# Performance work log

Hardware: AMD Instinct MI355X
Metric: run time of the kernel (lower is better)

## Reference

```python
import jax, jax.numpy as jnp
import numpy as np

E, D, H, B, S = 16, 1024, 256, 4, 4096  # num_splats, model_dim, ff_dim//num_splats, batch, seq_len


def setup_inputs() -> dict:
    key = jax.random.key(0)
    ks = jax.random.split(key, 8)
    s = 0.02  # init scale for stability
    return {
        "x": jax.random.normal(ks[0], (B, S, D), dtype=jnp.float32),
        "splat_id": jax.random.randint(ks[1], (S,), 0, E, dtype=jnp.int32),
        "W1": jax.random.normal(ks[2], (E, D, H), dtype=jnp.float32) * s,
        "b1": jnp.zeros((E, H), dtype=jnp.float32),
        "W2": jax.random.normal(ks[3], (E, H, D), dtype=jnp.float32) * s,
        "b2": jnp.zeros((E, D), dtype=jnp.float32),
        "Wg1": jax.random.normal(ks[4], (D, D), dtype=jnp.float32) * s,
        "bg1": jnp.zeros((D,), dtype=jnp.float32),
        "Wg2": jax.random.normal(ks[5], (D, D), dtype=jnp.float32) * s,
        "bg2": jnp.zeros((D,), dtype=jnp.float32),
    }


def reference(x, splat_id, W1, b1, W2, b2, Wg1, bg1, Wg2, bg2):
    # Splat-aware dispatch: token s is processed by expert splat_id[s].
    # Equivalent vectorized form: run every expert's small MLP, mask at the
    # hidden layer by expert assignment, and sum over experts (each token is
    # assigned to exactly one expert, matching the gather->MLP->scatter loop).
    nE = W1.shape[0]
    onehot = (splat_id[None, :] == jnp.arange(nE, dtype=splat_id.dtype)[:, None]).astype(x.dtype)  # [E,S]
    # hidden: [E,B,S,H]
    h = jax.nn.gelu(jnp.einsum('bsd,edh->ebsh', x, W1) + b1[:, None, None, :], approximate=False)
    h = h * onehot[:, None, :, None]  # zero tokens not routed to expert e
    routed = jnp.einsum('ebsh,ehd->bsd', h, W2)  # [B,S,D]
    routed = routed + jnp.einsum('es,ed->sd', onehot, b2)[None, :, :]  # per-token expert bias
    # global aggregator MLP (torch GELU default = exact erf form)
    g = jax.nn.gelu(routed @ Wg1 + bg1, approximate=False)
    return g @ Wg2 + bg2
```

## Files before the change

kernel.cpp:

```cpp
#include <hip/hip_runtime.h>


#define DEV __device__ __forceinline__

typedef float f32x4 __attribute__((ext_vector_type(4)));
typedef short short8 __attribute__((ext_vector_type(8)));

DEV unsigned short f2bf(float f) {
  unsigned u = __float_as_uint(f);
  u += 0x7fffu + ((u >> 16) & 1u);
  return (unsigned short)(u >> 16);
}

DEV void gload_lds16(const void* g, void* l) {
  __builtin_amdgcn_global_load_lds(
      (const __attribute__((address_space(1))) unsigned int*)g,
      (__attribute__((address_space(3))) unsigned int*)l, 16, 0, 0);
}

DEV float gelu_exact(float v) {
  return 0.5f * v * (1.0f + erff(v * 0.70710678118654752f));
}

__global__ __launch_bounds__(256) void cast_bf16_kernel(
    const float* __restrict__ in, unsigned short* __restrict__ out, long n) {
  long i = ((long)blockIdx.x * 256 + threadIdx.x) * 8;
  if (i >= n) return;
  float4 v0 = *(const float4*)(in + i);
  float4 v1 = *(const float4*)(in + i + 4);
  uint4 o;
  o.x = (unsigned)f2bf(v0.x) | ((unsigned)f2bf(v0.y) << 16);
  o.y = (unsigned)f2bf(v0.z) | ((unsigned)f2bf(v0.w) << 16);
  o.z = (unsigned)f2bf(v1.x) | ((unsigned)f2bf(v1.y) << 16);
  o.w = (unsigned)f2bf(v1.z) | ((unsigned)f2bf(v1.w) << 16);
  *(uint4*)(out + i) = o;
}

__global__ __launch_bounds__(256) void tcast_kernel(
    const float* __restrict__ in, unsigned short* __restrict__ out,
    int R, int C, long stride) {
  __shared__ float tile[64][65];
  const int t = threadIdx.x;
  const long base = (long)blockIdx.z * stride;
  const int r0 = blockIdx.y * 64, c0 = blockIdx.x * 64;
  const int cc = t & 63, rr = t >> 6;
#pragma unroll
  for (int i = 0; i < 16; i++) {
    int r = rr + i * 4;
    tile[r][cc] = in[base + (long)(r0 + r) * C + (c0 + cc)];
  }
  __syncthreads();
#pragma unroll
  for (int i = 0; i < 16; i++) {
    int c = rr + i * 4;
    out[base + (long)(c0 + c) * R + (r0 + cc)] = f2bf(tile[cc][c]);
  }
}

__global__ __launch_bounds__(256) void route_kernel(
    const int* __restrict__ sid, int S, int* __restrict__ offs, int* __restrict__ order) {
  __shared__ int cnt[16], cur[16];
  const int t = threadIdx.x;
  if (t < 16) cnt[t] = 0;
  __syncthreads();
  for (int s = t; s < S; s += 256) atomicAdd(&cnt[sid[s]], 1);
  __syncthreads();
  if (t == 0) {
    int a = 0;
    for (int e = 0; e < 16; e++) { offs[e] = a; cur[e] = a; a += cnt[e]; }
    offs[16] = a;
  }
  __syncthreads();
  for (int s = t; s < S; s += 256) {
    int p = atomicAdd(&cur[sid[s]], 1);
    order[p] = s;
  }
}

template <bool GATHER_A, bool SCATTER_C, bool GELU, bool OUT_F32>
__global__ __launch_bounds__(256) void gemm_mfma(
    const unsigned short* __restrict__ A, const unsigned short* __restrict__ BT,
    const float* __restrict__ bias, void* __restrict__ Cout,
    int M, int N, int K,
    const int* __restrict__ order, const int* __restrict__ offs,
    int S, long btStride, int biasStride) {
  const int t = (int)threadIdx.x;
  const int lane = t & 63;
  const int w = t >> 6;
  const int wm = w >> 1, wn = w & 1;
  const int tileN = (int)blockIdx.x, tileM = (int)blockIdx.y, e = (int)blockIdx.z;

  const int o0 = offs[e], o1 = offs[e + 1];
  const int rowBase = 4 * o0;
  const int Me = 4 * (o1 - o0);
  if (tileM * 128 >= Me) return;
  const unsigned short* bt = BT + (long)e * btStride;
  const float* bs = bias + (long)e * biasStride;

  __shared__ __align__(16) unsigned short lA[128 * 64];
  __shared__ __align__(16) unsigned short lB[128 * 64];

  const unsigned short* aSrc[4];
  const unsigned short* bSrc[4];
  {
    const int q = t & 7;
#pragma unroll
    for (int i = 0; i < 4; i++) {
      const int row = i * 32 + (t >> 3);
      const int koff = ((q * 16) ^ ((row & 7) << 4)) >> 1;
      long arow;
      const int lrow = tileM * 128 + row;
      const int rr = (lrow < Me) ? lrow : (Me - 1);
      const int g = rowBase + rr;
      if (GATHER_A) {
        const int s = order[g >> 2];
        arow = (long)(g & 3) * S + s;
      } else {
        arow = g;
      }
      aSrc[i] = A + arow * (long)K + koff;
      const int col = tileN * 128 + row;
      bSrc[i] = bt + (long)col * K + koff;
    }
  }

  f32x4 acc[4][4] = {};

  const int KT = K >> 6;
  for (int kt = 0; kt < KT; kt++) {
    __syncthreads();
#pragma unroll
    for (int i = 0; i < 4; i++) {
      gload_lds16(aSrc[i] + (kt << 6), (void*)(lA + i * 2048 + w * 512));
      gload_lds16(bSrc[i] + (kt << 6), (void*)(lB + i * 2048 + w * 512));
    }
    __syncthreads();
#pragma unroll
    for (int kk = 0; kk < 2; kk++) {
      short8 af[4], bfr[4];
      const int kbyte = kk * 64 + (lane >> 4) * 16;
#pragma unroll
      for (int mi = 0; mi < 4; mi++) {
        const int row = wm * 64 + mi * 16 + (lane & 15);
        const int off = row * 128 + (kbyte ^ ((row & 7) << 4));
        af[mi] = *(const short8*)((const char*)lA + off);
      }
#pragma unroll
      for (int ni = 0; ni < 4; ni++) {
        const int row = wn * 64 + ni * 16 + (lane & 15);
        const int off = row * 128 + (kbyte ^ ((row & 7) << 4));
        bfr[ni] = *(const short8*)((const char*)lB + off);
      }
#pragma unroll
      for (int mi = 0; mi < 4; mi++)
#pragma unroll
        for (int ni = 0; ni < 4; ni++)
          acc[mi][ni] = __builtin_amdgcn_mfma_f32_16x16x32_bf16(af[mi], bfr[ni], acc[mi][ni], 0, 0, 0);
    }
  }

  float bcol[4];
#pragma unroll
  for (int ni = 0; ni < 4; ni++)
    bcol[ni] = bs[tileN * 128 + wn * 64 + ni * 16 + (lane & 15)];

#pragma unroll
  for (int mi = 0; mi < 4; mi++) {
#pragma unroll
    for (int j = 0; j < 4; j++) {
      const int lrow = tileM * 128 + wm * 64 + mi * 16 + ((lane >> 4) * 4) + j;
      if (lrow >= Me) continue;
      const int g = rowBase + lrow;
      long crow;
      if (SCATTER_C) crow = (long)(g & 3) * S + order[g >> 2];
      else crow = g;
#pragma unroll
      for (int ni = 0; ni < 4; ni++) {
        float v = acc[mi][ni][j] + bcol[ni];
        if (GELU) v = gelu_exact(v);
        const long cidx = crow * (long)N + tileN * 128 + wn * 64 + ni * 16 + (lane & 15);
        if (OUT_F32) ((float*)Cout)[cidx] = v;
        else ((unsigned short*)Cout)[cidx] = f2bf(v);
      }
    }
  }
}

template <bool GELU, bool OUT_F32>
__global__ __launch_bounds__(512, 2) void gemm_dense256(
    const unsigned short* __restrict__ A, const unsigned short* __restrict__ BT,
    const float* __restrict__ bias, void* __restrict__ Cout,
    int N, int K, int ntiles) {
  __shared__ __align__(16) unsigned short lds[3 * (256 * 64 + 128 * 64)];
  unsigned short* ldsA = lds;
  unsigned short* ldsB = lds + 3 * 16384;

  const int t = (int)threadIdx.x;
  const int lane = t & 63;
  const int w = t >> 6;
  const int wm = w >> 1;
  const int wn = w & 1;

  const int cpx = (int)gridDim.x >> 3;
  const int swz = ((int)blockIdx.x & 7) * cpx + ((int)blockIdx.x >> 3);
  const int mtile = swz / ntiles, ntile = swz % ntiles;

  const int koff = (((t & 7) * 16) ^ (((t >> 3) & 7) << 4)) >> 1;
  const unsigned short* aSrc[4];
  const unsigned short* bSrc[2];
#pragma unroll
  for (int i = 0; i < 4; i++)
    aSrc[i] = A + (long)(mtile * 256 + i * 64 + (t >> 3)) * K + koff;
#pragma unroll
  for (int i = 0; i < 2; i++)
    bSrc[i] = BT + (long)(ntile * 128 + i * 64 + (t >> 3)) * K + koff;
  const int dstOff = (t >> 3) * 64 + (t & 7) * 8;

  const int KT = K >> 6;

  auto STAGE = [&](int kt, int bi) {
    unsigned short* ba = ldsA + bi * 16384 + dstOff;
    unsigned short* bb = ldsB + bi * 8192 + dstOff;
    const long ko = (long)kt << 6;
#pragma unroll
    for (int i = 0; i < 4; i++) gload_lds16(aSrc[i] + ko, ba + i * 4096);
#pragma unroll
    for (int i = 0; i < 2; i++) gload_lds16(bSrc[i] + ko, bb + i * 4096);
  };

  f32x4 acc[4][4] = {};

  STAGE(0, 0);
  STAGE(1, 1);

  for (int kt = 0; kt < KT; kt++) {
    const int rd = kt % 3;
    if (kt + 2 < KT) {
      STAGE(kt + 2, (kt + 2) % 3);
      asm volatile("s_waitcnt vmcnt(12)" ::: "memory");
    } else if (kt + 1 < KT) {
      asm volatile("s_waitcnt vmcnt(6)" ::: "memory");
    } else {
      asm volatile("s_waitcnt vmcnt(0)" ::: "memory");
    }
    asm volatile("s_barrier" ::: "memory");

    const unsigned short* ba = ldsA + rd * 16384;
    const unsigned short* bb = ldsB + rd * 8192;
#pragma unroll
    for (int kk = 0; kk < 2; kk++) {
      short8 af[4], bfr[4];
      const int kb = kk * 64 + ((lane >> 4) << 4);
      const int sw = (lane & 7) << 4;
#pragma unroll
      for (int mi = 0; mi < 4; mi++) {
        const int row = wm * 64 + mi * 16 + (lane & 15);
        af[mi] = *(const short8*)((const char*)ba + row * 128 + (kb ^ sw));
      }
#pragma unroll
      for (int ni = 0; ni < 4; ni++) {
        const int row = wn * 64 + ni * 16 + (lane & 15);
        bfr[ni] = *(const short8*)((const char*)bb + row * 128 + (kb ^ sw));
      }
      __builtin_amdgcn_s_setprio(1);
#pragma unroll
      for (int mi = 0; mi < 4; mi++)
#pragma unroll
        for (int ni = 0; ni < 4; ni++)
          acc[mi][ni] = __builtin_amdgcn_mfma_f32_16x16x32_bf16(af[mi], bfr[ni], acc[mi][ni], 0, 0, 0);
      __builtin_amdgcn_s_setprio(0);
    }
    asm volatile("s_waitcnt lgkmcnt(0)" ::: "memory");
    asm volatile("s_barrier" ::: "memory");
  }

  float bcol[4];
#pragma unroll
  for (int ni = 0; ni < 4; ni++)
    bcol[ni] = bias[ntile * 128 + wn * 64 + ni * 16 + (lane & 15)];

#pragma unroll
  for (int mi = 0; mi < 4; mi++) {
#pragma unroll
    for (int j = 0; j < 4; j++) {
      const long crow = mtile * 256 + wm * 64 + mi * 16 + ((lane >> 4) * 4) + j;
#pragma unroll
      for (int ni = 0; ni < 4; ni++) {
        float v = acc[mi][ni][j] + bcol[ni];
        if (GELU) v = gelu_exact(v);
        const long cidx = crow * (long)N + ntile * 128 + wn * 64 + ni * 16 + (lane & 15);
        if (OUT_F32) ((float*)Cout)[cidx] = v;
        else ((unsigned short*)Cout)[cidx] = f2bf(v);
      }
    }
  }
}

extern "C" void kernel_launch(void* const* d_in, const int* in_sizes, int n_in,
                              void* d_out, int out_size, void* d_ws, size_t ws_size,
                              hipStream_t stream) {
  const float* x   = (const float*)d_in[0];
  const int*   sid = (const int*)d_in[1];
  const float* W1  = (const float*)d_in[2];
  const float* b1  = (const float*)d_in[3];
  const float* W2  = (const float*)d_in[4];
  const float* b2  = (const float*)d_in[5];
  const float* Wg1 = (const float*)d_in[6];
  const float* bg1 = (const float*)d_in[7];
  const float* Wg2 = (const float*)d_in[8];
  const float* bg2 = (const float*)d_in[9];
  (void)in_sizes; (void)n_in; (void)out_size; (void)ws_size;

  constexpr int E = 16, D = 1024, H = 256, S = 4096, B = 4;
  constexpr long NT = (long)B * S;

  char* ws = (char*)d_ws;
  unsigned short* xb   = (unsigned short*)(ws);
  unsigned short* w1t  = (unsigned short*)(ws + 33554432);
  unsigned short* w2t  = (unsigned short*)(ws + 41943040);
  unsigned short* wg1t = (unsigned short*)(ws + 50331648);
  unsigned short* wg2t = (unsigned short*)(ws + 52428800);
  unsigned short* hbuf = (unsigned short*)(ws + 54525952);
  unsigned short* rout = (unsigned short*)(ws + 62914560);
  int* offs  = (int*)(ws + 96468992);
  int* order = (int*)(ws + 96469248);

  cast_bf16_kernel<<<dim3((unsigned)(NT * D / 2048)), 256, 0, stream>>>(x, xb, NT * D);
  tcast_kernel<<<dim3(H / 64, D / 64, E), 256, 0, stream>>>(W1, w1t, D, H, (long)D * H);
  tcast_kernel<<<dim3(D / 64, H / 64, E), 256, 0, stream>>>(W2, w2t, H, D, (long)D * H);
  tcast_kernel<<<dim3(D / 64, D / 64, 1), 256, 0, stream>>>(Wg1, wg1t, D, D, (long)D * D);
  tcast_kernel<<<dim3(D / 64, D / 64, 1), 256, 0, stream>>>(Wg2, wg2t, D, D, (long)D * D);
  route_kernel<<<1, 256, 0, stream>>>(sid, S, offs, order);

  gemm_mfma<true, false, true, false><<<dim3(H / 128, 128, E), 256, 0, stream>>>(
      xb, w1t, b1, hbuf, (int)NT, H, D, order, offs, S, (long)H * D, H);
  gemm_mfma<false, true, false, false><<<dim3(D / 128, 128, E), 256, 0, stream>>>(
      hbuf, w2t, b2, rout, (int)NT, D, H, order, offs, S, (long)D * H, D);
  gemm_dense256<true, false><<<dim3((unsigned)(NT / 256) * (D / 128)), 512, 0, stream>>>(
      rout, wg1t, bg1, xb, D, D, D / 128);
  gemm_dense256<false, true><<<dim3((unsigned)(NT / 256) * (D / 128)), 512, 0, stream>>>(
      xb, wg2t, bg2, d_out, D, D, D / 128);
}
```

Measured before the change: 208.3 us.

## Replace dense aggregator GEMM with 256x256-tile 8-phase pipelined kernel

Rewrites the two dense aggregator GEMMs to use 256x256 output tiles with a 4x2... wait wm=w>>2 gives 2x4 wave layout, each wave computing 128x64. Loads are split into half-tiles staged through an 8-slot LDS ring with interleaved global->LDS copies, LDS reads and MFMA phases separated by barriers. The aim is higher arithmetic intensity per block and finer overlap of memory loads with matrix math. It halves the grid size, uses more registers per thread, and adds many barriers, which may reduce occupancy or introduce synchronization overhead.

```diff
diff --git a/kernel.cpp b/kernel.cpp
--- a/kernel.cpp
+++ b/kernel.cpp
@@ -21,6 +21,11 @@
 DEV float gelu_exact(float v) {
   return 0.5f * v * (1.0f + erff(v * 0.70710678118654752f));
 }
+
+#define BARRIER() __builtin_amdgcn_s_barrier()
+#define LGKM0()   asm volatile("s_waitcnt lgkmcnt(0)" ::: "memory")
+#define VMW(n)    asm volatile("s_waitcnt vmcnt(" #n ")" ::: "memory")
+#define SB0()     __builtin_amdgcn_sched_barrier(0)
 
 __global__ __launch_bounds__(256) void cast_bf16_kernel(
     const float* __restrict__ in, unsigned short* __restrict__ out, long n) {
@@ -187,108 +192,154 @@
 }
 
 template <bool GELU, bool OUT_F32>
-__global__ __launch_bounds__(512, 2) void gemm_dense256(
+__global__ __launch_bounds__(512, 2) void gemm_8phase(
     const unsigned short* __restrict__ A, const unsigned short* __restrict__ BT,
     const float* __restrict__ bias, void* __restrict__ Cout,
     int N, int K, int ntiles) {
-  __shared__ __align__(16) unsigned short lds[3 * (256 * 64 + 128 * 64)];
-  unsigned short* ldsA = lds;
-  unsigned short* ldsB = lds + 3 * 16384;
+  __shared__ __align__(16) unsigned short lds[8 * 8192];
 
   const int t = (int)threadIdx.x;
   const int lane = t & 63;
   const int w = t >> 6;
-  const int wm = w >> 1;
-  const int wn = w & 1;
+  const int wm = w >> 2;
+  const int wn = w & 3;
 
   const int cpx = (int)gridDim.x >> 3;
   const int swz = ((int)blockIdx.x & 7) * cpx + ((int)blockIdx.x >> 3);
   const int mtile = swz / ntiles, ntile = swz % ntiles;
 
-  const int koff = (((t & 7) * 16) ^ (((t >> 3) & 7) << 4)) >> 1;
-  const unsigned short* aSrc[4];
-  const unsigned short* bSrc[2];
-#pragma unroll
-  for (int i = 0; i < 4; i++)
-    aSrc[i] = A + (long)(mtile * 256 + i * 64 + (t >> 3)) * K + koff;
-#pragma unroll
-  for (int i = 0; i < 2; i++)
-    bSrc[i] = BT + (long)(ntile * 128 + i * 64 + (t >> 3)) * K + koff;
-  const int dstOff = (t >> 3) * 64 + (t & 7) * 8;
+  const int tq = t & 7;
+  const unsigned short* srcA[2][2];
+  const unsigned short* srcB[2][2];
+#pragma unroll
+  for (int i = 0; i < 2; i++) {
+    const int ir = i * 64 + (t >> 3);
+    const int koffE = ((tq * 16) ^ ((ir & 7) << 4)) >> 1;
+#pragma unroll
+    for (int h = 0; h < 2; h++) {
+      const int ra = (ir & 63) + (h << 6) + ((ir >> 6) << 7);
+      srcA[i][h] = A + (long)(mtile * 256 + ra) * K + koffE;
+      const int cb = (ir & 31) + (h << 5) + ((ir >> 5) << 6);
+      srcB[i][h] = BT + (long)(ntile * 256 + cb) * K + koffE;
+    }
+  }
+  const int dstE = (t >> 3) * 64 + tq * 8;
+
+  auto STAGE = [&](int d, int mat, int h, int kt) {
+    unsigned short* dst = lds + ((d * 4 + mat * 2 + h) << 13) + dstE;
+    const unsigned short* s0 = (mat == 0 ? srcA[0][h] : srcB[0][h]) + (kt << 6);
+    const unsigned short* s1 = (mat == 0 ? srcA[1][h] : srcB[1][h]) + (kt << 6);
+    gload_lds16(s0, dst);
+    gload_lds16(s1, dst + 4096);
+  };
+
+  short8 aReg[8], bReg[8];
+  const int klane = (lane >> 4) << 4;
+  const int rsw = (lane & 7) << 4;
+
+  auto LDA = [&](int d, int mh) {
+    const char* base = (const char*)(lds + ((d * 4 + mh) << 13));
+    const int r0 = wm * 64 + (lane & 15);
+#pragma unroll
+    for (int m = 0; m < 4; m++) {
+      const int row = r0 + m * 16;
+#pragma unroll
+      for (int kk = 0; kk < 2; kk++)
+        aReg[m * 2 + kk] = *(const short8*)(base + row * 128 + ((kk * 64 + klane) ^ rsw));
+    }
+  };
+  auto LDB = [&](int d, int nh) {
+    const char* base = (const char*)(lds + ((d * 4 + 2 + nh) << 13));
+    const int r0 = wn * 32 + (lane & 15);
+#pragma unroll
+    for (int n = 0; n < 2; n++) {
+      const int row = r0 + n * 16;
+#pragma unroll
+      for (int kk = 0; kk < 2; kk++)
+        bReg[(nh * 2 + n) * 2 + kk] = *(const short8*)(base + row * 128 + ((kk * 64 + klane) ^ rsw));
+    }
+  };
+
+  f32x4 acc[8][4] = {};
+  auto MMA = [&](int mb, int nb) {
+    __builtin_amdgcn_s_setprio(1);
+#pragma unroll
+    for (int kk = 0; kk < 2; kk++)
+#pragma unroll
+      for (int m = 0; m < 4; m++)
+#pragma unroll
+        for (int n = 0; n < 2; n++)
+          acc[mb + m][nb + n] = __builtin_amdgcn_mfma_f32_16x16x32_bf16(
+              aReg[m * 2 + kk], bReg[(nb + n) * 2 + kk], acc[mb + m][nb + n], 0, 0, 0);
+    __builtin_amdgcn_s_setprio(0);
+  };
 
   const int KT = K >> 6;
 
-  auto STAGE = [&](int kt, int bi) {
-    unsigned short* ba = ldsA + bi * 16384 + dstOff;
-    unsigned short* bb = ldsB + bi * 8192 + dstOff;
-    const long ko = (long)kt << 6;
-#pragma unroll
-    for (int i = 0; i < 4; i++) gload_lds16(aSrc[i] + ko, ba + i * 4096);
-#pragma unroll
-    for (int i = 0; i < 2; i++) gload_lds16(bSrc[i] + ko, bb + i * 4096);
-  };
-
-  f32x4 acc[4][4] = {};
-
-  STAGE(0, 0);
-  STAGE(1, 1);
-
-  for (int kt = 0; kt < KT; kt++) {
-    const int rd = kt % 3;
-    if (kt + 2 < KT) {
-      STAGE(kt + 2, (kt + 2) % 3);
-      asm volatile("s_waitcnt vmcnt(12)" ::: "memory");
-    } else if (kt + 1 < KT) {
-      asm volatile("s_waitcnt vmcnt(6)" ::: "memory");
-    } else {
-      asm volatile("s_waitcnt vmcnt(0)" ::: "memory");
-    }
-    asm volatile("s_barrier" ::: "memory");
-
-    const unsigned short* ba = ldsA + rd * 16384;
-    const unsigned short* bb = ldsB + rd * 8192;
-#pragma unroll
-    for (int kk = 0; kk < 2; kk++) {
-      short8 af[4], bfr[4];
-      const int kb = kk * 64 + ((lane >> 4) << 4);
-      const int sw = (lane & 7) << 4;
-#pragma unroll
-      for (int mi = 0; mi < 4; mi++) {
-        const int row = wm * 64 + mi * 16 + (lane & 15);
-        af[mi] = *(const short8*)((const char*)ba + row * 128 + (kb ^ sw));
-      }
-#pragma unroll
-      for (int ni = 0; ni < 4; ni++) {
-        const int row = wn * 64 + ni * 16 + (lane & 15);
-        bfr[ni] = *(const short8*)((const char*)bb + row * 128 + (kb ^ sw));
-      }
-      __builtin_amdgcn_s_setprio(1);
-#pragma unroll
-      for (int mi = 0; mi < 4; mi++)
-#pragma unroll
-        for (int ni = 0; ni < 4; ni++)
-          acc[mi][ni] = __builtin_amdgcn_mfma_f32_16x16x32_bf16(af[mi], bfr[ni], acc[mi][ni], 0, 0, 0);
-      __builtin_amdgcn_s_setprio(0);
-    }
-    asm volatile("s_waitcnt lgkmcnt(0)" ::: "memory");
-    asm volatile("s_barrier" ::: "memory");
-  }
+  {
+    const int t1 = (KT > 1) ? 1 : 0;
+    STAGE(0, 0, 0, 0); STAGE(0, 1, 0, 0); STAGE(0, 1, 1, 0); STAGE(0, 0, 1, 0);
+    STAGE(1, 0, 0, t1); STAGE(1, 1, 0, t1); STAGE(1, 1, 1, t1);
+    VMW(6);
+    BARRIER(); SB0();
+  }
+
+  for (int it = 0; it < (KT >> 1); ++it) {
+    const int tb = (2 * it + 1 < KT) ? 2 * it + 1 : KT - 1;
+    int nx = 2 * it + 2; if (nx >= KT) nx = KT - 1;
+    int ny = 2 * it + 3; if (ny >= KT) ny = KT - 1;
+    LDA(0, 0); LDB(0, 0); STAGE(1, 0, 1, tb);
+    BARRIER(); LGKM0(); SB0();
+    MMA(0, 0);
+    BARRIER(); SB0();
+    LDB(0, 1); STAGE(0, 0, 0, nx);
+    BARRIER(); LGKM0(); SB0();
+    MMA(0, 2);
+    BARRIER(); SB0();
+    LDA(0, 1); STAGE(0, 1, 0, nx);
+    BARRIER(); LGKM0(); SB0();
+    MMA(4, 0);
+    BARRIER(); SB0();
+    STAGE(0, 1, 1, nx);
+    BARRIER(); LGKM0(); SB0();
+    MMA(4, 2);
+    VMW(4);
+    BARRIER(); SB0();
+    LDA(1, 0); LDB(1, 0); STAGE(0, 0, 1, nx);
+    BARRIER(); LGKM0(); SB0();
+    MMA(0, 0);
+    BARRIER(); SB0();
+    LDB(1, 1); STAGE(1, 0, 0, ny);
+    BARRIER(); LGKM0(); SB0();
+    MMA(0, 2);
+    BARRIER(); SB0();
+    LDA(1, 1); STAGE(1, 1, 0, ny);
+    BARRIER(); LGKM0(); SB0();
+    MMA(4, 0);
+    BARRIER(); SB0();
+    STAGE(1, 1, 1, ny);
+    BARRIER(); LGKM0(); SB0();
+    MMA(4, 2);
+    VMW(4);
+    BARRIER(); SB0();
+  }
+  VMW(0);
 
   float bcol[4];
 #pragma unroll
-  for (int ni = 0; ni < 4; ni++)
-    bcol[ni] = bias[ntile * 128 + wn * 64 + ni * 16 + (lane & 15)];
-
-#pragma unroll
-  for (int mi = 0; mi < 4; mi++) {
+  for (int n = 0; n < 4; n++)
+    bcol[n] = bias[ntile * 256 + wn * 64 + n * 16 + (lane & 15)];
+  const int cbase = ntile * 256 + wn * 64 + (lane & 15);
+#pragma unroll
+  for (int m = 0; m < 8; m++) {
 #pragma unroll
     for (int j = 0; j < 4; j++) {
-      const long crow = mtile * 256 + wm * 64 + mi * 16 + ((lane >> 4) * 4) + j;
-#pragma unroll
-      for (int ni = 0; ni < 4; ni++) {
-        float v = acc[mi][ni][j] + bcol[ni];
+      const long crow = mtile * 256 + wm * 128 + m * 16 + ((lane >> 4) << 2) + j;
+#pragma unroll
+      for (int n = 0; n < 4; n++) {
+        float v = acc[m][n][j] + bcol[n];
         if (GELU) v = gelu_exact(v);
-        const long cidx = crow * (long)N + ntile * 128 + wn * 64 + ni * 16 + (lane & 15);
+        const long cidx = crow * (long)N + cbase + n * 16;
         if (OUT_F32) ((float*)Cout)[cidx] = v;
         else ((unsigned short*)Cout)[cidx] = f2bf(v);
       }
@@ -336,8 +387,8 @@
       xb, w1t, b1, hbuf, (int)NT, H, D, order, offs, S, (long)H * D, H);
   gemm_mfma<false, true, false, false><<<dim3(D / 128, 128, E), 256, 0, stream>>>(
       hbuf, w2t, b2, rout, (int)NT, D, H, order, offs, S, (long)D * H, D);
-  gemm_dense256<true, false><<<dim3((unsigned)(NT / 256) * (D / 128)), 512, 0, stream>>>(
-      rout, wg1t, bg1, xb, D, D, D / 128);
-  gemm_dense256<false, true><<<dim3((unsigned)(NT / 256) * (D / 128)), 512, 0, stream>>>(
-      xb, wg2t, bg2, d_out, D, D, D / 128);
-}
+  gemm_8phase<true, false><<<dim3((unsigned)(NT / 256) * (D / 256)), 512, 0, stream>>>(
+      rout, wg1t, bg1, xb, D, D, D / 256);
+  gemm_8phase<false, true><<<dim3((unsigned)(NT / 256) * (D / 256)), 512, 0, stream>>>(
+      xb, wg2t, bg2, d_out, D, D, D / 256);
+}
```

Result: faster. 192.9 us (-7.4%).
